# Optimization experiments

Hardware: AMD Instinct MI355X
Metric: run time of the kernel (lower is better)

## Reference

```python
import jax, jax.numpy as jnp
import numpy as np

B, S, F, D, H, L = 32768, 32, 10, 64, 4, 2
HD = D // H  # head_dim = 16
DFF = 2 * D  # ffn hidden = 128
DH = D // 2  # head hidden = 32


def _ln(x, g, b, eps=1e-5):
    mu = jnp.mean(x, axis=-1, keepdims=True)
    var = jnp.mean((x - mu) ** 2, axis=-1, keepdims=True)
    return (x - mu) * jax.lax.rsqrt(var + eps) * g + b


def setup_inputs() -> dict:
    key = jax.random.key(0)
    ks = jax.random.split(key, 16)
    r = lambda k, shp, s=0.05: jax.random.normal(k, shp, dtype=jnp.float32) * s
    return {
        "x": jax.random.normal(ks[0], (B, S, F), dtype=jnp.float32),
        "w_in": r(ks[1], (F, D)), "b_in": jnp.zeros((D,), jnp.float32),
        "pos": r(ks[2], (S, D)),
        "wq": r(ks[3], (L, D, D)), "wk": r(ks[4], (L, D, D)), "wv": r(ks[5], (L, D, D)),
        "wo": r(ks[6], (L, D, D)), "bo": jnp.zeros((L, D), jnp.float32),
        "g1": jnp.ones((L, D), jnp.float32), "be1": jnp.zeros((L, D), jnp.float32),
        "g2": jnp.ones((L, D), jnp.float32), "be2": jnp.zeros((L, D), jnp.float32),
        "w1": r(ks[7], (L, D, DFF)), "b1": jnp.zeros((L, DFF), jnp.float32),
        "w2": r(ks[8], (L, DFF, D)), "b2": jnp.zeros((L, D), jnp.float32),
        "hw1": r(ks[9], (D, DH)), "hb1": jnp.zeros((DH,), jnp.float32),
        "hw2": r(ks[10], (DH, 1)), "hb2": jnp.zeros((1,), jnp.float32),
    }


def reference(x, w_in, b_in, pos, wq, wk, wv, wo, bo, g1, be1, g2, be2,
              w1, b1, w2, b2, hw1, hb1, hw2, hb2):
    b, s, _ = x.shape
    h = x @ w_in + b_in + pos[None, :s]  # [B,S,D]
    scale = 1.0 / np.sqrt(HD)
    for i in range(L):
        # --- attention sublayer (pre-LN) ---
        hn = _ln(h, g1[i], be1[i])
        q = (hn @ wq[i]).reshape(b, s, H, HD)
        k = (hn @ wk[i]).reshape(b, s, H, HD)
        v = (hn @ wv[i]).reshape(b, s, H, HD)
        scores = jnp.einsum('bqhd,bkhd->bhqk', q, k) * scale
        attn = jax.nn.softmax(scores, axis=-1)
        ctx = jnp.einsum('bhqk,bkhd->bqhd', attn, v).reshape(b, s, D)
        h = h + ctx @ wo[i] + bo[i]
        # --- FFN sublayer (pre-LN) ---
        hn = _ln(h, g2[i], be2[i])
        h = h + jax.nn.relu(hn @ w1[i] + b1[i]) @ w2[i] + b2[i]
    pooled = h.mean(axis=1)  # [B,D]
    out = jax.nn.relu(pooled @ hw1 + hb1) @ hw2 + hb2
    return jnp.tanh(out)  # [B,1]
```

## Files before the change

### kernel.cpp

```cpp
#include <hip/hip_runtime.h>
#include <cmath>

typedef _Float16 h8_t __attribute__((ext_vector_type(8)));
typedef float f4_t __attribute__((ext_vector_type(4)));

constexpr int Bsz = 32768, S = 32, F = 10, Dm = 64, Ln = 2, DFF = 128;
constexpr int ZP = 72;
constexpr int VP = 40;
constexpr int NB = 2;

constexpr int ZONE_H = S * ZP;
constexpr int VT_H   = Dm * VP;
constexpr int SMEM_H = NB * (ZONE_H + VT_H);

constexpr int NFRAG = 4 + Ln * 64;
constexpr size_t PB_OFF = (size_t)NFRAG * 512 * 2;

__global__ __launch_bounds__(256, 2)
void prep_kernel(const float* __restrict__ w_in, const float* __restrict__ b_in,
                 const float* __restrict__ pos,
                 const float* __restrict__ wq, const float* __restrict__ wk,
                 const float* __restrict__ wv, const float* __restrict__ wo,
                 const float* __restrict__ w1, const float* __restrict__ w2,
                 _Float16* __restrict__ wsf, float* __restrict__ pbf) {
  int gid = blockIdx.x * 256 + threadIdx.x;
  int lane = gid & 63;
  int l15 = lane & 15, lk8 = (lane >> 4) << 3;
  if (gid < NFRAG * 64) {
    int frag = gid >> 6;
    float vals[8];
    if (frag < 4) {
      int n = 16 * frag + l15;
      #pragma unroll
      for (int j = 0; j < 8; ++j) {
        int k = lk8 + j;
        vals[j] = (k < F) ? w_in[k * Dm + n] : 0.f;
      }
    } else {
      int f = frag - 4;
      int layer = f >> 6; f &= 63;
      const float* W; int ncols, n, kbase;
      if (f < 32) {
        int sub = f >> 3, g = f & 7;
        int nt = g & 3, kt = g >> 2;
        W = ((sub == 0) ? wk : (sub == 1) ? wv : (sub == 2) ? wq : wo) + layer * Dm * Dm;
        ncols = Dm; n = 16 * nt + l15; kbase = kt * 32 + lk8;
      } else if (f < 48) {
        int g = f - 32, nt = g & 7, kt = g >> 3;
        W = w1 + layer * Dm * DFF; ncols = DFF; n = 16 * nt + l15; kbase = kt * 32 + lk8;
      } else {
        int g = f - 48, nt = g & 3, kt = g >> 2;
        W = w2 + layer * DFF * Dm; ncols = Dm; n = 16 * nt + l15; kbase = kt * 32 + lk8;
      }
      #pragma unroll
      for (int j = 0; j < 8; ++j) vals[j] = W[(kbase + j) * ncols + n];
    }
    h8_t o;
    #pragma unroll
    for (int j = 0; j < 8; ++j) o[j] = (_Float16)vals[j];
    *(h8_t*)&wsf[(size_t)gid * 8] = o;
  } else if (gid < NFRAG * 64 + 8 * 64) {
    int r = gid - NFRAG * 64;
    int pb = r >> 6;
    int mt = pb >> 2, nt = pb & 3;
    int row = 16 * mt + ((lane >> 4) << 2);
    int col = 16 * nt + l15;
    f4_t v;
    #pragma unroll
    for (int q = 0; q < 4; ++q) v[q] = pos[(row + q) * Dm + col] + b_in[col];
    *(f4_t*)&pbf[(size_t)r * 4] = v;
  }
}

__global__ __launch_bounds__(128, 4)
void tlob_kernel(const float* __restrict__ x,
                 const float* __restrict__ g1, const float* __restrict__ be1,
                 const float* __restrict__ g2, const float* __restrict__ be2,
                 const float* __restrict__ bo, const float* __restrict__ b1,
                 const float* __restrict__ b2, const float* __restrict__ hw1,
                 const float* __restrict__ hb1, const float* __restrict__ hw2,
                 const float* __restrict__ hb2,
                 const _Float16* __restrict__ wsf, const float* __restrict__ pbf,
                 float* __restrict__ out) {
  __shared__ __align__(16) _Float16 smem[SMEM_H];
  const int tid = threadIdx.x;
  const int lane = tid & 63;
  const int wid = tid >> 6;
  const int elem = blockIdx.x * NB + wid;

  _Float16* zone = smem + wid * ZONE_H;
  _Float16* vT = smem + NB * ZONE_H + wid * VT_H;

  const int l15 = lane & 15;
  const int G = lane >> 4;
  const int lk8 = G << 3;
  const int r0b = G << 2;
  const int swzR = ((l15 >> 2) & 3) << 3;
  int col4[4];
  #pragma unroll
  for (int nt = 0; nt < 4; ++nt) col4[nt] = l15 + 16 * nt;

  const h8_t* FR = (const h8_t*)wsf;
  auto ldf = [&](int f) -> h8_t { return FR[f * 64 + lane]; };

  f4_t z4; z4[0] = 0.f; z4[1] = 0.f; z4[2] = 0.f; z4[3] = 0.f;
  h8_t hz;
  #pragma unroll
  for (int j = 0; j < 8; ++j) hz[j] = (_Float16)0.f;

  auto mfma = [&](h8_t a, h8_t b, f4_t c) -> f4_t {
    return __builtin_amdgcn_mfma_f32_16x16x32_f16(a, b, c, 0, 0, 0);
  };
  auto cstore = [&](_Float16* buf, int pitch, int mt, int col, f4_t v, float scale) {
    int c = col ^ lk8;
    int r = 16 * mt + r0b;
    #pragma unroll
    for (int q = 0; q < 4; ++q) buf[(r + q) * pitch + c] = (_Float16)(v[q] * scale);
  };
  auto zfrag = [&](int i1, int i2) -> h8_t {
    return *(const h8_t*)&zone[(l15 + 16 * i1) * ZP + ((i2 * 32 + lk8) ^ swzR)];
  };

  h8_t xa[2];
  #pragma unroll
  for (int mt = 0; mt < 2; ++mt) {
    const float* xr = x + (size_t)elem * (S * F) + (16 * mt + l15) * F;
    h8_t v = hz;
    #pragma unroll
    for (int j = 0; j < 8; ++j) {
      int f = lk8 + j;
      if (f < F) v[j] = (_Float16)xr[f];
    }
    xa[mt] = v;
  }

  f4_t hacc[2][4];
  #pragma unroll
  for (int nt = 0; nt < 4; ++nt) {
    h8_t wb = ldf(nt);
    #pragma unroll
    for (int mt = 0; mt < 2; ++mt) {
      f4_t ini = *(const f4_t*)&pbf[((size_t)(mt * 4 + nt) * 64 + lane) * 4];
      hacc[mt][nt] = mfma(xa[mt], wb, ini);
    }
  }

  auto doLN = [&](const float* g, const float* be, h8_t fr[2][2]) {
    float gv[4], bv[4];
    #pragma unroll
    for (int nt = 0; nt < 4; ++nt) { gv[nt] = g[col4[nt]]; bv[nt] = be[col4[nt]]; }
    #pragma unroll
    for (int mt = 0; mt < 2; ++mt) {
      f4_t ps = hacc[mt][0] + hacc[mt][1] + hacc[mt][2] + hacc[mt][3];
      f4_t pq = hacc[mt][0] * hacc[mt][0] + hacc[mt][1] * hacc[mt][1] +
                hacc[mt][2] * hacc[mt][2] + hacc[mt][3] * hacc[mt][3];
      #pragma unroll
      for (int m = 1; m <= 8; m <<= 1) {
        #pragma unroll
        for (int q = 0; q < 4; ++q) {
          ps[q] += __shfl_xor(ps[q], m);
          pq[q] += __shfl_xor(pq[q], m);
        }
      }
      f4_t muv, rsv;
      #pragma unroll
      for (int q = 0; q < 4; ++q) {
        float mu = ps[q] * (1.f / 64.f);
        float var = pq[q] * (1.f / 64.f) - mu * mu;
        muv[q] = mu; rsv[q] = rsqrtf(var + 1e-5f);
      }
      #pragma unroll
      for (int nt = 0; nt < 4; ++nt) {
        int c = col4[nt] ^ lk8;
        int r = 16 * mt + r0b;
        #pragma unroll
        for (int q = 0; q < 4; ++q) {
          float hn = (hacc[mt][nt][q] - muv[q]) * rsv[q] * gv[nt] + bv[nt];
          zone[(r + q) * ZP + c] = (_Float16)hn;
        }
      }
    }
    #pragma unroll
    for (int i1 = 0; i1 < 2; ++i1)
      #pragma unroll
      for (int i2 = 0; i2 < 2; ++i2) fr[i1][i2] = zfrag(i1, i2);
  };

  #pragma unroll 1
  for (int layer = 0; layer < Ln; ++layer) {
    const int fb = 4 + layer * 64;
    float bov[4];
    #pragma unroll
    for (int nt = 0; nt < 4; ++nt) bov[nt] = bo[layer * Dm + col4[nt]];

    h8_t hnf[2][2];
    doLN(g1 + layer * Dm, be1 + layer * Dm, hnf);

    h8_t kA[2][2];
    {
      #pragma unroll
      for (int nt = 0; nt < 4; ++nt) {
        h8_t w0 = ldf(fb + 0 + 0 * 4 + nt), w1f = ldf(fb + 0 + 1 * 4 + nt);
        #pragma unroll
        for (int mt = 0; mt < 2; ++mt) {
          f4_t acc = mfma(hnf[mt][0], w0, z4);
          acc = mfma(hnf[mt][1], w1f, acc);
          cstore(zone, ZP, mt, col4[nt], acc, 1.f);
        }
      }
      #pragma unroll
      for (int i1 = 0; i1 < 2; ++i1)
        #pragma unroll
        for (int i2 = 0; i2 < 2; ++i2) kA[i1][i2] = zfrag(i1, i2);
    }

    #pragma unroll
    for (int mtd = 0; mtd < 4; ++mtd) {
      h8_t a0 = ldf(fb + 8 + 0 * 4 + mtd), a1 = ldf(fb + 8 + 1 * 4 + mtd);
      #pragma unroll
      for (int nts = 0; nts < 2; ++nts) {
        f4_t acc = mfma(a0, hnf[nts][0], z4);
        acc = mfma(a1, hnf[nts][1], acc);
        cstore(vT, VP, mtd, l15 + 16 * nts, acc, 1.f);
      }
    }

    h8_t qf[2][2];
    {
      #pragma unroll
      for (int nt = 0; nt < 4; ++nt) {
        h8_t w0 = ldf(fb + 16 + 0 * 4 + nt), w1f = ldf(fb + 16 + 1 * 4 + nt);
        #pragma unroll
        for (int mt = 0; mt < 2; ++mt) {
          f4_t acc = mfma(hnf[mt][0], w0, z4);
          acc = mfma(hnf[mt][1], w1f, acc);
          cstore(zone, ZP, mt, col4[nt], acc, 0.25f);
        }
      }
      #pragma unroll
      for (int i1 = 0; i1 < 2; ++i1)
        #pragma unroll
        for (int i2 = 0; i2 < 2; ++i2) qf[i1][i2] = zfrag(i1, i2);
    }

    f4_t ctxf[2][4];
    #pragma unroll
    for (int hd = 0; hd < 4; ++hd) {
      const int kt = hd >> 1;
      bool keep = ((hd & 1) == 0) ? (lane < 32) : (lane >= 32);
      h8_t a0 = keep ? kA[0][kt] : hz;
      h8_t a1 = keep ? kA[1][kt] : hz;
      f4_t p[2][2];
      #pragma unroll
      for (int nq = 0; nq < 2; ++nq) {
        p[0][nq] = mfma(a0, qf[nq][kt], z4);
        p[1][nq] = mfma(a1, qf[nq][kt], z4);
      }
      #pragma unroll
      for (int nq = 0; nq < 2; ++nq) {
        #pragma unroll
        for (int mk = 0; mk < 2; ++mk)
          #pragma unroll
          for (int q = 0; q < 4; ++q) p[mk][nq][q] = __expf(p[mk][nq][q]);
        f4_t s4 = p[0][nq] + p[1][nq];
        float sm = s4[0] + s4[1] + s4[2] + s4[3];
        sm += __shfl_xor(sm, 16);
        sm += __shfl_xor(sm, 32);
        float inv = __builtin_amdgcn_rcpf(sm);
        #pragma unroll
        for (int mk = 0; mk < 2; ++mk)
          #pragma unroll
          for (int q = 0; q < 4; ++q) p[mk][nq][q] *= inv;
      }
      #pragma unroll
      for (int nq = 0; nq < 2; ++nq)
        #pragma unroll
        for (int mk = 0; mk < 2; ++mk)
          #pragma unroll
          for (int q = 0; q < 4; ++q)
            zone[(16 * nq + l15) * ZP + ((16 * mk + r0b + q) ^ swzR)] =
                (_Float16)p[mk][nq][q];
      h8_t pA0 = zfrag(0, 0), pA1 = zfrag(1, 0);
      h8_t vB = *(const h8_t*)&vT[(hd * 16 + l15) * VP + (lk8 ^ swzR)];
      ctxf[0][hd] = mfma(pA0, vB, z4);
      ctxf[1][hd] = mfma(pA1, vB, z4);
    }

    #pragma unroll
    for (int mt = 0; mt < 2; ++mt)
      #pragma unroll
      for (int hd = 0; hd < 4; ++hd) cstore(zone, ZP, mt, col4[hd], ctxf[mt][hd], 1.f);
    h8_t ca[2][2];
    #pragma unroll
    for (int i1 = 0; i1 < 2; ++i1)
      #pragma unroll
      for (int i2 = 0; i2 < 2; ++i2) ca[i1][i2] = zfrag(i1, i2);
    #pragma unroll
    for (int nt = 0; nt < 4; ++nt) {
      h8_t w0 = ldf(fb + 24 + 0 * 4 + nt), w1f = ldf(fb + 24 + 1 * 4 + nt);
      #pragma unroll
      for (int mt = 0; mt < 2; ++mt) {
        f4_t acc = mfma(ca[mt][0], w0, hacc[mt][nt]);
        acc = mfma(ca[mt][1], w1f, acc);
        #pragma unroll
        for (int q = 0; q < 4; ++q) hacc[mt][nt][q] = acc[q] + bov[nt];
      }
    }

    h8_t hn2f[2][2];
    doLN(g2 + layer * Dm, be2 + layer * Dm, hn2f);
    #pragma unroll 1
    for (int hf = 0; hf < 2; ++hf) {
      #pragma unroll
      for (int ntl = 0; ntl < 4; ++ntl) {
        int ntg = hf * 4 + ntl;
        h8_t w0 = ldf(fb + 32 + 0 * 8 + ntg), w1f = ldf(fb + 32 + 1 * 8 + ntg);
        float b1v = b1[layer * DFF + hf * 64 + col4[ntl]];
        f4_t bb; bb[0] = b1v; bb[1] = b1v; bb[2] = b1v; bb[3] = b1v;
        #pragma unroll
        for (int mt = 0; mt < 2; ++mt) {
          f4_t acc = mfma(hn2f[mt][0], w0, bb);
          acc = mfma(hn2f[mt][1], w1f, acc);
          #pragma unroll
          for (int q = 0; q < 4; ++q) acc[q] = fmaxf(acc[q], 0.f);
          cstore(zone, ZP, mt, col4[ntl], acc, 1.f);
        }
      }
      h8_t rf[2][2];
      #pragma unroll
      for (int i1 = 0; i1 < 2; ++i1)
        #pragma unroll
        for (int i2 = 0; i2 < 2; ++i2) rf[i1][i2] = zfrag(i1, i2);
      #pragma unroll
      for (int nt = 0; nt < 4; ++nt) {
        h8_t w0 = ldf(fb + 48 + (hf * 2 + 0) * 4 + nt);
        h8_t w1f = ldf(fb + 48 + (hf * 2 + 1) * 4 + nt);
        #pragma unroll
        for (int mt = 0; mt < 2; ++mt) {
          f4_t acc = mfma(rf[mt][0], w0, hacc[mt][nt]);
          hacc[mt][nt] = mfma(rf[mt][1], w1f, acc);
        }
      }
    }
    #pragma unroll
    for (int mt = 0; mt < 2; ++mt)
      #pragma unroll
      for (int nt = 0; nt < 4; ++nt) {
        float b2v = b2[layer * Dm + col4[nt]];
        #pragma unroll
        for (int q = 0; q < 4; ++q) hacc[mt][nt][q] += b2v;
      }
  }

  {
    float* pf = (float*)zone;
    #pragma unroll
    for (int nt = 0; nt < 4; ++nt) {
      float s = 0.f;
      #pragma unroll
      for (int mt = 0; mt < 2; ++mt)
        #pragma unroll
        for (int q = 0; q < 4; ++q) s += hacc[mt][nt][q];
      s += __shfl_xor(s, 16);
      s += __shfl_xor(s, 32);
      pf[col4[nt]] = s * (1.f / 32.f);
    }
    int j = lane & 31;
    float r = hb1[j];
    #pragma unroll
    for (int dd = 0; dd < 64; ++dd) r = fmaf(pf[dd], hw1[dd * 32 + j], r);
    r = fmaxf(r, 0.f);
    float t = r * hw2[j];
    t += __shfl_xor(t, 1); t += __shfl_xor(t, 2); t += __shfl_xor(t, 4);
    t += __shfl_xor(t, 8); t += __shfl_xor(t, 16);
    if (lane == 0) out[elem] = tanhf(t + hb2[0]);
  }
}

extern "C" void kernel_launch(void* const* d_in, const int* in_sizes, int n_in,
                              void* d_out, int out_size, void* d_ws, size_t ws_size,
                              hipStream_t stream) {
  (void)in_sizes; (void)n_in; (void)ws_size; (void)out_size;
  const float* x    = (const float*)d_in[0];
  const float* w_in = (const float*)d_in[1];
  const float* b_in = (const float*)d_in[2];
  const float* pos  = (const float*)d_in[3];
  const float* wq   = (const float*)d_in[4];
  const float* wk   = (const float*)d_in[5];
  const float* wv   = (const float*)d_in[6];
  const float* wo   = (const float*)d_in[7];
  const float* bo   = (const float*)d_in[8];
  const float* g1   = (const float*)d_in[9];
  const float* be1  = (const float*)d_in[10];
  const float* g2   = (const float*)d_in[11];
  const float* be2  = (const float*)d_in[12];
  const float* w1   = (const float*)d_in[13];
  const float* b1   = (const float*)d_in[14];
  const float* w2   = (const float*)d_in[15];
  const float* b2   = (const float*)d_in[16];
  const float* hw1  = (const float*)d_in[17];
  const float* hb1  = (const float*)d_in[18];
  const float* hw2  = (const float*)d_in[19];
  const float* hb2  = (const float*)d_in[20];
  float* out = (float*)d_out;

  _Float16* wsf = (_Float16*)d_ws;
  float* pbf = (float*)((char*)d_ws + PB_OFF);

  hipLaunchKernelGGL(prep_kernel, dim3(35), dim3(256), 0, stream,
                     w_in, b_in, pos, wq, wk, wv, wo, w1, w2, wsf, pbf);
  hipLaunchKernelGGL(tlob_kernel, dim3(Bsz / NB), dim3(128), 0, stream,
                     x, g1, be1, g2, be2, bo, b1, b2, hw1, hb1, hw2, hb2,
                     (const _Float16*)wsf, (const float*)pbf, out);
}
```

Baseline: 564.5 us.

## Keep activations in registers via transposed MFMA layout and cross-lane repacking

Transposes the activation layout so the channel dimension sits in the MFMA M operand, then converts accumulator fragments into operand fragments with lane shuffles, not round trips through shared memory. This removes the per-wave LDS zone and vT buffers, along with their stores, loads and swizzling. It also prepacks LayerNorm and bias vectors per lane in the prep kernel, folds the query scale into the packed weights, and moves to 4 waves per block. The cost is many more cross-lane shuffles and higher register pressure, which may limit occupancy.

```diff
diff --git a/kernel.cpp b/kernel.cpp
--- a/kernel.cpp
+++ b/kernel.cpp
@@ -2,30 +2,32 @@
 #include <cmath>
 
 typedef _Float16 h8_t __attribute__((ext_vector_type(8)));
+typedef _Float16 h2_t __attribute__((ext_vector_type(2)));
 typedef float f4_t __attribute__((ext_vector_type(4)));
+typedef unsigned int u32x4 __attribute__((ext_vector_type(4)));
 
 constexpr int Bsz = 32768, S = 32, F = 10, Dm = 64, Ln = 2, DFF = 128;
-constexpr int ZP = 72;
-constexpr int VP = 40;
-constexpr int NB = 2;
-
-constexpr int ZONE_H = S * ZP;
-constexpr int VT_H   = Dm * VP;
-constexpr int SMEM_H = NB * (ZONE_H + VT_H);
+constexpr int NB = 4;
 
 constexpr int NFRAG = 4 + Ln * 64;
-constexpr size_t PB_OFF = (size_t)NFRAG * 512 * 2;
+constexpr size_t PBF_OFF = (size_t)NFRAG * 512 * 2;
+constexpr size_t CPK_OFF = PBF_OFF + (size_t)8 * 64 * 16;
 
 __global__ __launch_bounds__(256, 2)
 void prep_kernel(const float* __restrict__ w_in, const float* __restrict__ b_in,
                  const float* __restrict__ pos,
                  const float* __restrict__ wq, const float* __restrict__ wk,
                  const float* __restrict__ wv, const float* __restrict__ wo,
-                 const float* __restrict__ w1, const float* __restrict__ w2,
-                 _Float16* __restrict__ wsf, float* __restrict__ pbf) {
+                 const float* __restrict__ bo, const float* __restrict__ g1,
+                 const float* __restrict__ be1, const float* __restrict__ g2,
+                 const float* __restrict__ be2, const float* __restrict__ w1,
+                 const float* __restrict__ b1, const float* __restrict__ w2,
+                 const float* __restrict__ b2,
+                 _Float16* __restrict__ wsf, float* __restrict__ pbf,
+                 float* __restrict__ cpk) {
   int gid = blockIdx.x * 256 + threadIdx.x;
   int lane = gid & 63;
-  int l15 = lane & 15, lk8 = (lane >> 4) << 3;
+  int l15 = lane & 15, lk8 = (lane >> 4) << 3, r0b = (lane >> 4) << 2;
   if (gid < NFRAG * 64) {
     int frag = gid >> 6;
     float vals[8];
@@ -39,11 +41,12 @@
     } else {
       int f = frag - 4;
       int layer = f >> 6; f &= 63;
-      const float* W; int ncols, n, kbase;
+      const float* W; int ncols, n, kbase; float scale = 1.f;
       if (f < 32) {
         int sub = f >> 3, g = f & 7;
         int nt = g & 3, kt = g >> 2;
         W = ((sub == 0) ? wk : (sub == 1) ? wv : (sub == 2) ? wq : wo) + layer * Dm * Dm;
+        if (sub == 2) scale = 0.25f;
         ncols = Dm; n = 16 * nt + l15; kbase = kt * 32 + lk8;
       } else if (f < 48) {
         int g = f - 32, nt = g & 7, kt = g >> 3;
@@ -53,327 +56,336 @@
         W = w2 + layer * DFF * Dm; ncols = Dm; n = 16 * nt + l15; kbase = kt * 32 + lk8;
       }
       #pragma unroll
-      for (int j = 0; j < 8; ++j) vals[j] = W[(kbase + j) * ncols + n];
+      for (int j = 0; j < 8; ++j) vals[j] = W[(kbase + j) * ncols + n] * scale;
     }
     h8_t o;
     #pragma unroll
     for (int j = 0; j < 8; ++j) o[j] = (_Float16)vals[j];
     *(h8_t*)&wsf[(size_t)gid * 8] = o;
-  } else if (gid < NFRAG * 64 + 8 * 64) {
+  } else if (gid < NFRAG * 64 + 512) {
     int r = gid - NFRAG * 64;
-    int pb = r >> 6;
-    int mt = pb >> 2, nt = pb & 3;
-    int row = 16 * mt + ((lane >> 4) << 2);
-    int col = 16 * nt + l15;
+    int p = r >> 6;
+    int ct = p >> 1, st = p & 1;
+    int seq = l15 + 16 * st;
     f4_t v;
     #pragma unroll
-    for (int q = 0; q < 4; ++q) v[q] = pos[(row + q) * Dm + col] + b_in[col];
+    for (int q = 0; q < 4; ++q) {
+      int ch = 16 * ct + r0b + q;
+      v[q] = pos[seq * Dm + ch] + b_in[ch];
+    }
     *(f4_t*)&pbf[(size_t)r * 4] = v;
-  }
-}
-
-__global__ __launch_bounds__(128, 4)
+  } else if (gid < NFRAG * 64 + 512 + Ln * 32 * 64) {
+    int r = gid - NFRAG * 64 - 512;
+    int layer = r >> 11;
+    int rr = r & 2047;
+    int fi = rr >> 6;
+    f4_t v;
+    if (fi < 24) {
+      int which = fi >> 2, ct = fi & 3;
+      const float* arr[6] = {g1, be1, g2, be2, bo, b2};
+      const float* src = arr[which] + layer * Dm;
+      #pragma unroll
+      for (int q = 0; q < 4; ++q) v[q] = src[16 * ct + r0b + q];
+    } else {
+      int dt = fi - 24;
+      const float* src = b1 + layer * DFF;
+      #pragma unroll
+      for (int q = 0; q < 4; ++q) v[q] = src[16 * dt + r0b + q];
+    }
+    *(f4_t*)&cpk[((size_t)(layer * 32 + fi) * 64 + lane) * 4] = v;
+  }
+}
+
+__device__ __forceinline__ f4_t mfma16(h8_t a, h8_t b, f4_t c) {
+  return __builtin_amdgcn_mfma_f32_16x16x32_f16(a, b, c, 0, 0, 0);
+}
+__device__ __forceinline__ unsigned pk2_rne(float a, float b) {
+  h2_t r; r[0] = (_Float16)a; r[1] = (_Float16)b;
+  return __builtin_bit_cast(unsigned, r);
+}
+__device__ __forceinline__ unsigned pk2_rtz(float a, float b) {
+  return __builtin_bit_cast(unsigned, __builtin_amdgcn_cvt_pkrtz(a, b));
+}
+template <bool RTZ>
+__device__ __forceinline__ h8_t repackF(f4_t lo, f4_t hi, int srcA, int srcB,
+                                        bool hiG) {
+  unsigned lo01 = RTZ ? pk2_rtz(lo[0], lo[1]) : pk2_rne(lo[0], lo[1]);
+  unsigned lo23 = RTZ ? pk2_rtz(lo[2], lo[3]) : pk2_rne(lo[2], lo[3]);
+  unsigned hi01 = RTZ ? pk2_rtz(hi[0], hi[1]) : pk2_rne(hi[0], hi[1]);
+  unsigned hi23 = RTZ ? pk2_rtz(hi[2], hi[3]) : pk2_rne(hi[2], hi[3]);
+  unsigned a0 = __shfl((int)lo01, srcA), a1 = __shfl((int)lo23, srcA);
+  unsigned b0 = __shfl((int)hi01, srcA), b1 = __shfl((int)hi23, srcA);
+  unsigned c0 = __shfl((int)lo01, srcB), c1 = __shfl((int)lo23, srcB);
+  unsigned d0 = __shfl((int)hi01, srcB), d1 = __shfl((int)hi23, srcB);
+  u32x4 r;
+  r[0] = hiG ? b0 : a0;
+  r[1] = hiG ? b1 : a1;
+  r[2] = hiG ? d0 : c0;
+  r[3] = hiG ? d1 : c1;
+  return __builtin_bit_cast(h8_t, r);
+}
+__device__ __forceinline__ void doLN(const f4_t (&h)[4][2], const f4_t (&gp)[4],
+                                     const f4_t (&bp)[4], h8_t (&hF)[2][2],
+                                     int srcA, int srcB, bool hiG) {
+  #pragma unroll
+  for (int st = 0; st < 2; ++st) {
+    f4_t s = h[0][st] + h[1][st] + h[2][st] + h[3][st];
+    f4_t s2 = h[0][st] * h[0][st] + h[1][st] * h[1][st] +
+              h[2][st] * h[2][st] + h[3][st] * h[3][st];
+    float sum = s[0] + s[1] + s[2] + s[3];
+    float sq  = s2[0] + s2[1] + s2[2] + s2[3];
+    sum += __shfl_xor(sum, 16); sum += __shfl_xor(sum, 32);
+    sq  += __shfl_xor(sq, 16);  sq  += __shfl_xor(sq, 32);
+    float mu = sum * (1.f / 64.f);
+    float var = sq * (1.f / 64.f) - mu * mu;
+    float rs = rsqrtf(var + 1e-5f);
+    f4_t hn[4];
+    #pragma unroll
+    for (int ct = 0; ct < 4; ++ct) {
+      #pragma unroll
+      for (int q = 0; q < 4; ++q)
+        hn[ct][q] = (h[ct][st][q] - mu) * rs * gp[ct][q] + bp[ct][q];
+    }
+    hF[0][st] = repackF<false>(hn[0], hn[1], srcA, srcB, hiG);
+    hF[1][st] = repackF<false>(hn[2], hn[3], srcA, srcB, hiG);
+  }
+}
+
+__global__ __launch_bounds__(256, 3)
 void tlob_kernel(const float* __restrict__ x,
-                 const float* __restrict__ g1, const float* __restrict__ be1,
-                 const float* __restrict__ g2, const float* __restrict__ be2,
-                 const float* __restrict__ bo, const float* __restrict__ b1,
-                 const float* __restrict__ b2, const float* __restrict__ hw1,
-                 const float* __restrict__ hb1, const float* __restrict__ hw2,
-                 const float* __restrict__ hb2,
+                 const float* __restrict__ hw1, const float* __restrict__ hb1,
+                 const float* __restrict__ hw2, const float* __restrict__ hb2,
                  const _Float16* __restrict__ wsf, const float* __restrict__ pbf,
-                 float* __restrict__ out) {
-  __shared__ __align__(16) _Float16 smem[SMEM_H];
-  const int tid = threadIdx.x;
-  const int lane = tid & 63;
-  const int wid = tid >> 6;
+                 const float* __restrict__ cpk, float* __restrict__ out) {
+  __shared__ float pfs[NB][64];
+  const int tid = threadIdx.x, lane = tid & 63, wid = tid >> 6;
   const int elem = blockIdx.x * NB + wid;
-
-  _Float16* zone = smem + wid * ZONE_H;
-  _Float16* vT = smem + NB * ZONE_H + wid * VT_H;
-
-  const int l15 = lane & 15;
-  const int G = lane >> 4;
-  const int lk8 = G << 3;
-  const int r0b = G << 2;
-  const int swzR = ((l15 >> 2) & 3) << 3;
-  int col4[4];
-  #pragma unroll
-  for (int nt = 0; nt < 4; ++nt) col4[nt] = l15 + 16 * nt;
+  const int l15 = lane & 15, G = lane >> 4;
+  const int lk8 = G << 3, r0b = G << 2;
+  const int srcA = (((2 * G) & 3) << 4) | l15;
+  const int srcB = (((2 * G + 1) & 3) << 4) | l15;
+  const bool hiG = (lane >= 32);
 
   const h8_t* FR = (const h8_t*)wsf;
+  const f4_t* PB = (const f4_t*)pbf;
+  const f4_t* CP = (const f4_t*)cpk;
   auto ldf = [&](int f) -> h8_t { return FR[f * 64 + lane]; };
+  auto ldc = [&](int layer, int fi) -> f4_t { return CP[(layer * 32 + fi) * 64 + lane]; };
 
   f4_t z4; z4[0] = 0.f; z4[1] = 0.f; z4[2] = 0.f; z4[3] = 0.f;
   h8_t hz;
   #pragma unroll
   for (int j = 0; j < 8; ++j) hz[j] = (_Float16)0.f;
 
-  auto mfma = [&](h8_t a, h8_t b, f4_t c) -> f4_t {
-    return __builtin_amdgcn_mfma_f32_16x16x32_f16(a, b, c, 0, 0, 0);
-  };
-  auto cstore = [&](_Float16* buf, int pitch, int mt, int col, f4_t v, float scale) {
-    int c = col ^ lk8;
-    int r = 16 * mt + r0b;
-    #pragma unroll
-    for (int q = 0; q < 4; ++q) buf[(r + q) * pitch + c] = (_Float16)(v[q] * scale);
-  };
-  auto zfrag = [&](int i1, int i2) -> h8_t {
-    return *(const h8_t*)&zone[(l15 + 16 * i1) * ZP + ((i2 * 32 + lk8) ^ swzR)];
-  };
-
-  h8_t xa[2];
+  h8_t xB[2];
   #pragma unroll
-  for (int mt = 0; mt < 2; ++mt) {
-    const float* xr = x + (size_t)elem * (S * F) + (16 * mt + l15) * F;
+  for (int st = 0; st < 2; ++st) {
+    const float* xr = x + (size_t)elem * (S * F) + (16 * st + l15) * F;
     h8_t v = hz;
     #pragma unroll
     for (int j = 0; j < 8; ++j) {
       int f = lk8 + j;
       if (f < F) v[j] = (_Float16)xr[f];
     }
-    xa[mt] = v;
-  }
-
-  f4_t hacc[2][4];
+    xB[st] = v;
+  }
+
+  f4_t hacc[4][2];
   #pragma unroll
-  for (int nt = 0; nt < 4; ++nt) {
-    h8_t wb = ldf(nt);
-    #pragma unroll
-    for (int mt = 0; mt < 2; ++mt) {
-      f4_t ini = *(const f4_t*)&pbf[((size_t)(mt * 4 + nt) * 64 + lane) * 4];
-      hacc[mt][nt] = mfma(xa[mt], wb, ini);
-    }
-  }
-
-  auto doLN = [&](const float* g, const float* be, h8_t fr[2][2]) {
-    float gv[4], bv[4];
-    #pragma unroll
-    for (int nt = 0; nt < 4; ++nt) { gv[nt] = g[col4[nt]]; bv[nt] = be[col4[nt]]; }
-    #pragma unroll
-    for (int mt = 0; mt < 2; ++mt) {
-      f4_t ps = hacc[mt][0] + hacc[mt][1] + hacc[mt][2] + hacc[mt][3];
-      f4_t pq = hacc[mt][0] * hacc[mt][0] + hacc[mt][1] * hacc[mt][1] +
-                hacc[mt][2] * hacc[mt][2] + hacc[mt][3] * hacc[mt][3];
-      #pragma unroll
-      for (int m = 1; m <= 8; m <<= 1) {
-        #pragma unroll
-        for (int q = 0; q < 4; ++q) {
-          ps[q] += __shfl_xor(ps[q], m);
-          pq[q] += __shfl_xor(pq[q], m);
-        }
-      }
-      f4_t muv, rsv;
-      #pragma unroll
-      for (int q = 0; q < 4; ++q) {
-        float mu = ps[q] * (1.f / 64.f);
-        float var = pq[q] * (1.f / 64.f) - mu * mu;
-        muv[q] = mu; rsv[q] = rsqrtf(var + 1e-5f);
-      }
-      #pragma unroll
-      for (int nt = 0; nt < 4; ++nt) {
-        int c = col4[nt] ^ lk8;
-        int r = 16 * mt + r0b;
-        #pragma unroll
-        for (int q = 0; q < 4; ++q) {
-          float hn = (hacc[mt][nt][q] - muv[q]) * rsv[q] * gv[nt] + bv[nt];
-          zone[(r + q) * ZP + c] = (_Float16)hn;
-        }
-      }
-    }
-    #pragma unroll
-    for (int i1 = 0; i1 < 2; ++i1)
-      #pragma unroll
-      for (int i2 = 0; i2 < 2; ++i2) fr[i1][i2] = zfrag(i1, i2);
-  };
+  for (int ct = 0; ct < 4; ++ct) {
+    h8_t wf = ldf(ct);
+    #pragma unroll
+    for (int st = 0; st < 2; ++st)
+      hacc[ct][st] = mfma16(wf, xB[st], PB[(ct * 2 + st) * 64 + lane]);
+  }
 
   #pragma unroll 1
   for (int layer = 0; layer < Ln; ++layer) {
     const int fb = 4 + layer * 64;
-    float bov[4];
-    #pragma unroll
-    for (int nt = 0; nt < 4; ++nt) bov[nt] = bo[layer * Dm + col4[nt]];
-
-    h8_t hnf[2][2];
-    doLN(g1 + layer * Dm, be1 + layer * Dm, hnf);
-
-    h8_t kA[2][2];
+
+    f4_t gp[4], bp[4];
+    #pragma unroll
+    for (int ct = 0; ct < 4; ++ct) { gp[ct] = ldc(layer, ct); bp[ct] = ldc(layer, 4 + ct); }
+    h8_t hnF[2][2];
+    doLN(hacc, gp, bp, hnF, srcA, srcB, hiG);
+
+    h8_t kF[2][2];
     {
+      f4_t kc[4][2];
+      #pragma unroll
+      for (int ot = 0; ot < 4; ++ot) {
+        h8_t w0 = ldf(fb + ot), w1 = ldf(fb + 4 + ot);
+        #pragma unroll
+        for (int st = 0; st < 2; ++st)
+          kc[ot][st] = mfma16(w1, hnF[1][st], mfma16(w0, hnF[0][st], z4));
+      }
+      #pragma unroll
+      for (int kt = 0; kt < 2; ++kt)
+        #pragma unroll
+        for (int st = 0; st < 2; ++st)
+          kF[kt][st] = repackF<false>(kc[2 * kt][st], kc[2 * kt + 1][st], srcA, srcB, hiG);
+    }
+    h8_t qF[2][2];
+    {
+      f4_t qc[4][2];
+      #pragma unroll
+      for (int ot = 0; ot < 4; ++ot) {
+        h8_t w0 = ldf(fb + 16 + ot), w1 = ldf(fb + 20 + ot);
+        #pragma unroll
+        for (int st = 0; st < 2; ++st)
+          qc[ot][st] = mfma16(w1, hnF[1][st], mfma16(w0, hnF[0][st], z4));
+      }
+      #pragma unroll
+      for (int kt = 0; kt < 2; ++kt)
+        #pragma unroll
+        for (int st = 0; st < 2; ++st)
+          qF[kt][st] = repackF<false>(qc[2 * kt][st], qc[2 * kt + 1][st], srcA, srcB, hiG);
+    }
+    h8_t vB[4];
+    {
+      f4_t vc[2][4];
       #pragma unroll
       for (int nt = 0; nt < 4; ++nt) {
-        h8_t w0 = ldf(fb + 0 + 0 * 4 + nt), w1f = ldf(fb + 0 + 1 * 4 + nt);
-        #pragma unroll
-        for (int mt = 0; mt < 2; ++mt) {
-          f4_t acc = mfma(hnf[mt][0], w0, z4);
-          acc = mfma(hnf[mt][1], w1f, acc);
-          cstore(zone, ZP, mt, col4[nt], acc, 1.f);
-        }
-      }
-      #pragma unroll
-      for (int i1 = 0; i1 < 2; ++i1)
-        #pragma unroll
-        for (int i2 = 0; i2 < 2; ++i2) kA[i1][i2] = zfrag(i1, i2);
-    }
-
-    #pragma unroll
-    for (int mtd = 0; mtd < 4; ++mtd) {
-      h8_t a0 = ldf(fb + 8 + 0 * 4 + mtd), a1 = ldf(fb + 8 + 1 * 4 + mtd);
-      #pragma unroll
-      for (int nts = 0; nts < 2; ++nts) {
-        f4_t acc = mfma(a0, hnf[nts][0], z4);
-        acc = mfma(a1, hnf[nts][1], acc);
-        cstore(vT, VP, mtd, l15 + 16 * nts, acc, 1.f);
-      }
-    }
-
-    h8_t qf[2][2];
-    {
-      #pragma unroll
-      for (int nt = 0; nt < 4; ++nt) {
-        h8_t w0 = ldf(fb + 16 + 0 * 4 + nt), w1f = ldf(fb + 16 + 1 * 4 + nt);
-        #pragma unroll
-        for (int mt = 0; mt < 2; ++mt) {
-          f4_t acc = mfma(hnf[mt][0], w0, z4);
-          acc = mfma(hnf[mt][1], w1f, acc);
-          cstore(zone, ZP, mt, col4[nt], acc, 0.25f);
-        }
-      }
-      #pragma unroll
-      for (int i1 = 0; i1 < 2; ++i1)
-        #pragma unroll
-        for (int i2 = 0; i2 < 2; ++i2) qf[i1][i2] = zfrag(i1, i2);
-    }
-
-    f4_t ctxf[2][4];
+        h8_t w0 = ldf(fb + 8 + nt), w1 = ldf(fb + 12 + nt);
+        #pragma unroll
+        for (int mt = 0; mt < 2; ++mt)
+          vc[mt][nt] = mfma16(hnF[1][mt], w1, mfma16(hnF[0][mt], w0, z4));
+      }
+      #pragma unroll
+      for (int nt = 0; nt < 4; ++nt)
+        vB[nt] = repackF<false>(vc[0][nt], vc[1][nt], srcA, srcB, hiG);
+    }
+
+    f4_t ctx[4][2];
     #pragma unroll
     for (int hd = 0; hd < 4; ++hd) {
       const int kt = hd >> 1;
-      bool keep = ((hd & 1) == 0) ? (lane < 32) : (lane >= 32);
-      h8_t a0 = keep ? kA[0][kt] : hz;
-      h8_t a1 = keep ? kA[1][kt] : hz;
+      bool keep = (hd & 1) ? (lane >= 32) : (lane < 32);
+      h8_t a0 = keep ? kF[kt][0] : hz;
+      h8_t a1 = keep ? kF[kt][1] : hz;
       f4_t p[2][2];
       #pragma unroll
-      for (int nq = 0; nq < 2; ++nq) {
-        p[0][nq] = mfma(a0, qf[nq][kt], z4);
-        p[1][nq] = mfma(a1, qf[nq][kt], z4);
-      }
-      #pragma unroll
-      for (int nq = 0; nq < 2; ++nq) {
+      for (int sq = 0; sq < 2; ++sq) {
+        p[0][sq] = mfma16(a0, qF[kt][sq], z4);
+        p[1][sq] = mfma16(a1, qF[kt][sq], z4);
+      }
+      #pragma unroll
+      for (int sq = 0; sq < 2; ++sq) {
         #pragma unroll
         for (int mk = 0; mk < 2; ++mk)
           #pragma unroll
-          for (int q = 0; q < 4; ++q) p[mk][nq][q] = __expf(p[mk][nq][q]);
-        f4_t s4 = p[0][nq] + p[1][nq];
-        float sm = s4[0] + s4[1] + s4[2] + s4[3];
+          for (int q = 0; q < 4; ++q) p[mk][sq][q] = __expf(p[mk][sq][q]);
+        f4_t t = p[0][sq] + p[1][sq];
+        float sm = t[0] + t[1] + t[2] + t[3];
         sm += __shfl_xor(sm, 16);
         sm += __shfl_xor(sm, 32);
         float inv = __builtin_amdgcn_rcpf(sm);
-        #pragma unroll
-        for (int mk = 0; mk < 2; ++mk)
+        f4_t plo, phi;
+        #pragma unroll
+        for (int q = 0; q < 4; ++q) { plo[q] = p[0][sq][q] * inv; phi[q] = p[1][sq][q] * inv; }
+        h8_t pF = repackF<true>(plo, phi, srcA, srcB, hiG);
+        ctx[hd][sq] = mfma16(vB[hd], pF, z4);
+      }
+    }
+
+    {
+      h8_t cF[2][2];
+      #pragma unroll
+      for (int st = 0; st < 2; ++st) {
+        cF[0][st] = repackF<false>(ctx[0][st], ctx[1][st], srcA, srcB, hiG);
+        cF[1][st] = repackF<false>(ctx[2][st], ctx[3][st], srcA, srcB, hiG);
+      }
+      f4_t bop[4];
+      #pragma unroll
+      for (int ct = 0; ct < 4; ++ct) bop[ct] = ldc(layer, 16 + ct);
+      #pragma unroll
+      for (int ot = 0; ot < 4; ++ot) {
+        h8_t w0 = ldf(fb + 24 + ot), w1 = ldf(fb + 28 + ot);
+        #pragma unroll
+        for (int st = 0; st < 2; ++st) {
+          f4_t acc = mfma16(w1, cF[1][st], mfma16(w0, cF[0][st], hacc[ot][st]));
           #pragma unroll
-          for (int q = 0; q < 4; ++q) p[mk][nq][q] *= inv;
-      }
-      #pragma unroll
-      for (int nq = 0; nq < 2; ++nq)
-        #pragma unroll
-        for (int mk = 0; mk < 2; ++mk)
-          #pragma unroll
-          for (int q = 0; q < 4; ++q)
-            zone[(16 * nq + l15) * ZP + ((16 * mk + r0b + q) ^ swzR)] =
-                (_Float16)p[mk][nq][q];
-      h8_t pA0 = zfrag(0, 0), pA1 = zfrag(1, 0);
-      h8_t vB = *(const h8_t*)&vT[(hd * 16 + l15) * VP + (lk8 ^ swzR)];
-      ctxf[0][hd] = mfma(pA0, vB, z4);
-      ctxf[1][hd] = mfma(pA1, vB, z4);
-    }
-
-    #pragma unroll
-    for (int mt = 0; mt < 2; ++mt)
-      #pragma unroll
-      for (int hd = 0; hd < 4; ++hd) cstore(zone, ZP, mt, col4[hd], ctxf[mt][hd], 1.f);
-    h8_t ca[2][2];
-    #pragma unroll
-    for (int i1 = 0; i1 < 2; ++i1)
-      #pragma unroll
-      for (int i2 = 0; i2 < 2; ++i2) ca[i1][i2] = zfrag(i1, i2);
-    #pragma unroll
-    for (int nt = 0; nt < 4; ++nt) {
-      h8_t w0 = ldf(fb + 24 + 0 * 4 + nt), w1f = ldf(fb + 24 + 1 * 4 + nt);
-      #pragma unroll
-      for (int mt = 0; mt < 2; ++mt) {
-        f4_t acc = mfma(ca[mt][0], w0, hacc[mt][nt]);
-        acc = mfma(ca[mt][1], w1f, acc);
-        #pragma unroll
-        for (int q = 0; q < 4; ++q) hacc[mt][nt][q] = acc[q] + bov[nt];
-      }
-    }
-
-    h8_t hn2f[2][2];
-    doLN(g2 + layer * Dm, be2 + layer * Dm, hn2f);
-    #pragma unroll 1
-    for (int hf = 0; hf < 2; ++hf) {
-      #pragma unroll
-      for (int ntl = 0; ntl < 4; ++ntl) {
-        int ntg = hf * 4 + ntl;
-        h8_t w0 = ldf(fb + 32 + 0 * 8 + ntg), w1f = ldf(fb + 32 + 1 * 8 + ntg);
-        float b1v = b1[layer * DFF + hf * 64 + col4[ntl]];
-        f4_t bb; bb[0] = b1v; bb[1] = b1v; bb[2] = b1v; bb[3] = b1v;
-        #pragma unroll
-        for (int mt = 0; mt < 2; ++mt) {
-          f4_t acc = mfma(hn2f[mt][0], w0, bb);
-          acc = mfma(hn2f[mt][1], w1f, acc);
+          for (int q = 0; q < 4; ++q) hacc[ot][st][q] = acc[q] + bop[ot][q];
+        }
+      }
+    }
+
+    #pragma unroll
+    for (int ct = 0; ct < 4; ++ct) { gp[ct] = ldc(layer, 8 + ct); bp[ct] = ldc(layer, 12 + ct); }
+    h8_t h2F[2][2];
+    doLN(hacc, gp, bp, h2F, srcA, srcB, hiG);
+    #pragma unroll
+    for (int half = 0; half < 2; ++half) {
+      f4_t a1c[4][2];
+      #pragma unroll
+      for (int otl = 0; otl < 4; ++otl) {
+        int ot = 4 * half + otl;
+        h8_t w0 = ldf(fb + 32 + ot), w1 = ldf(fb + 40 + ot);
+        f4_t b1p = ldc(layer, 24 + ot);
+        #pragma unroll
+        for (int st = 0; st < 2; ++st) {
+          f4_t acc = mfma16(w1, h2F[1][st], mfma16(w0, h2F[0][st], b1p));
           #pragma unroll
           for (int q = 0; q < 4; ++q) acc[q] = fmaxf(acc[q], 0.f);
-          cstore(zone, ZP, mt, col4[ntl], acc, 1.f);
+          a1c[otl][st] = acc;
         }
       }
-      h8_t rf[2][2];
-      #pragma unroll
-      for (int i1 = 0; i1 < 2; ++i1)
-        #pragma unroll
-        for (int i2 = 0; i2 < 2; ++i2) rf[i1][i2] = zfrag(i1, i2);
-      #pragma unroll
-      for (int nt = 0; nt < 4; ++nt) {
-        h8_t w0 = ldf(fb + 48 + (hf * 2 + 0) * 4 + nt);
-        h8_t w1f = ldf(fb + 48 + (hf * 2 + 1) * 4 + nt);
-        #pragma unroll
-        for (int mt = 0; mt < 2; ++mt) {
-          f4_t acc = mfma(rf[mt][0], w0, hacc[mt][nt]);
-          hacc[mt][nt] = mfma(rf[mt][1], w1f, acc);
-        }
-      }
-    }
-    #pragma unroll
-    for (int mt = 0; mt < 2; ++mt)
-      #pragma unroll
-      for (int nt = 0; nt < 4; ++nt) {
-        float b2v = b2[layer * Dm + col4[nt]];
-        #pragma unroll
-        for (int q = 0; q < 4; ++q) hacc[mt][nt][q] += b2v;
-      }
+      h8_t rF[2][2];
+      #pragma unroll
+      for (int ktl = 0; ktl < 2; ++ktl)
+        #pragma unroll
+        for (int st = 0; st < 2; ++st)
+          rF[ktl][st] = repackF<false>(a1c[2 * ktl][st], a1c[2 * ktl + 1][st], srcA, srcB, hiG);
+      #pragma unroll
+      for (int ot = 0; ot < 4; ++ot) {
+        h8_t w0 = ldf(fb + 48 + 4 * (2 * half + 0) + ot);
+        h8_t w1 = ldf(fb + 48 + 4 * (2 * half + 1) + ot);
+        #pragma unroll
+        for (int st = 0; st < 2; ++st)
+          hacc[ot][st] = mfma16(w1, rF[1][st], mfma16(w0, rF[0][st], hacc[ot][st]));
+      }
+    }
+    {
+      f4_t b2p[4];
+      #pragma unroll
+      for (int ct = 0; ct < 4; ++ct) b2p[ct] = ldc(layer, 20 + ct);
+      #pragma unroll
+      for (int ct = 0; ct < 4; ++ct)
+        #pragma unroll
+        for (int st = 0; st < 2; ++st)
+          #pragma unroll
+          for (int q = 0; q < 4; ++q) hacc[ct][st][q] += b2p[ct][q];
+    }
   }
 
   {
-    float* pf = (float*)zone;
-    #pragma unroll
-    for (int nt = 0; nt < 4; ++nt) {
-      float s = 0.f;
-      #pragma unroll
-      for (int mt = 0; mt < 2; ++mt)
-        #pragma unroll
-        for (int q = 0; q < 4; ++q) s += hacc[mt][nt][q];
-      s += __shfl_xor(s, 16);
-      s += __shfl_xor(s, 32);
-      pf[col4[nt]] = s * (1.f / 32.f);
+    float* pf = pfs[wid];
+    f4_t t[4];
+    #pragma unroll
+    for (int ct = 0; ct < 4; ++ct) t[ct] = hacc[ct][0] + hacc[ct][1];
+    #pragma unroll
+    for (int m = 1; m <= 8; m <<= 1) {
+      #pragma unroll
+      for (int ct = 0; ct < 4; ++ct)
+        #pragma unroll
+        for (int q = 0; q < 4; ++q) t[ct][q] += __shfl_xor(t[ct][q], m);
+    }
+    if (l15 == 0) {
+      #pragma unroll
+      for (int ct = 0; ct < 4; ++ct)
+        #pragma unroll
+        for (int q = 0; q < 4; ++q)
+          pf[16 * ct + r0b + q] = t[ct][q] * (1.f / 32.f);
     }
     int j = lane & 31;
     float r = hb1[j];
     #pragma unroll
     for (int dd = 0; dd < 64; ++dd) r = fmaf(pf[dd], hw1[dd * 32 + j], r);
     r = fmaxf(r, 0.f);
-    float t = r * hw2[j];
-    t += __shfl_xor(t, 1); t += __shfl_xor(t, 2); t += __shfl_xor(t, 4);
-    t += __shfl_xor(t, 8); t += __shfl_xor(t, 16);
-    if (lane == 0) out[elem] = tanhf(t + hb2[0]);
+    float tt = r * hw2[j];
+    tt += __shfl_xor(tt, 1); tt += __shfl_xor(tt, 2); tt += __shfl_xor(tt, 4);
+    tt += __shfl_xor(tt, 8); tt += __shfl_xor(tt, 16);
+    if (lane == 0) out[elem] = tanhf(tt + hb2[0]);
   }
 }
 
@@ -405,11 +417,13 @@
   float* out = (float*)d_out;
 
   _Float16* wsf = (_Float16*)d_ws;
-  float* pbf = (float*)((char*)d_ws + PB_OFF);
-
-  hipLaunchKernelGGL(prep_kernel, dim3(35), dim3(256), 0, stream,
-                     w_in, b_in, pos, wq, wk, wv, wo, w1, w2, wsf, pbf);
-  hipLaunchKernelGGL(tlob_kernel, dim3(Bsz / NB), dim3(128), 0, stream,
-                     x, g1, be1, g2, be2, bo, b1, b2, hw1, hb1, hw2, hb2,
-                     (const _Float16*)wsf, (const float*)pbf, out);
-}
+  float* pbf = (float*)((char*)d_ws + PBF_OFF);
+  float* cpk = (float*)((char*)d_ws + CPK_OFF);
+
+  hipLaunchKernelGGL(prep_kernel, dim3(51), dim3(256), 0, stream,
+                     w_in, b_in, pos, wq, wk, wv, wo, bo, g1, be1, g2, be2,
+                     w1, b1, w2, b2, wsf, pbf, cpk);
+  hipLaunchKernelGGL(tlob_kernel, dim3(Bsz / NB), dim3(256), 0, stream,
+                     x, hw1, hb1, hw2, hb2,
+                     (const _Float16*)wsf, (const float*)pbf, (const float*)cpk, out);
+}
```

Result: faster. 452.4 us (-19.8%).
